# Kernel optimization log

Hardware: AMD Instinct MI355X
Metric: run time of the kernel (lower is better)

## Reference

```python
import jax, jax.numpy as jnp
import numpy as np

D_MODEL = 1024
N_HEADS = 16
HEAD_DIM = D_MODEL // N_HEADS
D_FF = 4096


def setup_inputs() -> dict:
    key = jax.random.key(0)
    ks = jax.random.split(key, 16)
    s = 0.02
    x = jax.random.normal(ks[0], (4, 2048, D_MODEL), dtype=jnp.float32)
    p = {
        'x': x,
        'wq': jax.random.normal(ks[1], (D_MODEL, D_MODEL), jnp.float32) * s,
        'bq': jnp.zeros((D_MODEL,), jnp.float32),
        'wk': jax.random.normal(ks[2], (D_MODEL, D_MODEL), jnp.float32) * s,
        'bk': jnp.zeros((D_MODEL,), jnp.float32),
        'wv': jax.random.normal(ks[3], (D_MODEL, D_MODEL), jnp.float32) * s,
        'bv': jnp.zeros((D_MODEL,), jnp.float32),
        'wo': jax.random.normal(ks[4], (D_MODEL, D_MODEL), jnp.float32) * s,
        'bo': jnp.zeros((D_MODEL,), jnp.float32),
        'w1': jax.random.normal(ks[5], (D_MODEL, D_FF), jnp.float32) * s,
        'b1': jnp.zeros((D_FF,), jnp.float32),
        'w2': jax.random.normal(ks[6], (D_FF, D_MODEL), jnp.float32) * s,
        'b2': jnp.zeros((D_MODEL,), jnp.float32),
        'ln1_g': jnp.ones((D_MODEL,), jnp.float32),
        'ln1_b': jnp.zeros((D_MODEL,), jnp.float32),
        'ln2_g': jnp.ones((D_MODEL,), jnp.float32),
        'ln2_b': jnp.zeros((D_MODEL,), jnp.float32),
    }
    return p


def _layernorm(x, g, b, eps=1e-5):
    mu = jnp.mean(x, axis=-1, keepdims=True)
    var = jnp.mean(jnp.square(x - mu), axis=-1, keepdims=True)
    return (x - mu) * jax.lax.rsqrt(var + eps) * g + b


def reference(x, wq, bq, wk, bk, wv, bv, wo, bo, w1, b1, w2, b2, ln1_g, ln1_b, ln2_g, ln2_b):
    B, S, D = x.shape
    normed = _layernorm(x, ln1_g, ln1_b)
    # projections -> [B, H, S, Dh]
    def split_heads(t):
        return t.reshape(B, S, N_HEADS, HEAD_DIM).transpose(0, 2, 1, 3)
    q = split_heads(normed @ wq + bq)
    k = split_heads(normed @ wk + bk)
    v = split_heads(normed @ wv + bv)
    scale = 1.0 / jnp.sqrt(jnp.float32(HEAD_DIM))
    scores = jnp.einsum('bhqd,bhkd->bhqk', q, k) * scale  # [B,H,S,S]
    causal = jnp.tril(jnp.ones((S, S), dtype=bool))
    scores = jnp.where(causal[None, None], scores, -jnp.inf)
    probs = jax.nn.softmax(scores, axis=-1)
    attn = jnp.einsum('bhqk,bhkd->bhqd', probs, v)
    attn = attn.transpose(0, 2, 1, 3).reshape(B, S, D)
    x = x + (attn @ wo + bo)
    h = _layernorm(x, ln2_g, ln2_b)
    h = jax.nn.gelu(h @ w1 + b1, approximate=False)
    x = x + (h @ w2 + b2)
    return x
```

## Files before the change

### kernel.cpp

```cpp
#include <hip/hip_runtime.h>
#include <hip/hip_bf16.h>
#include <math.h>

typedef __attribute__((ext_vector_type(8))) short short8;
typedef __attribute__((ext_vector_type(4))) float floatx4;

#define D_MODEL 1024
#define N_HEADS 16
#define HEAD_DIM 64
#define D_FF 4096
#define BATCH 4
#define SEQ 2048
#define NTOK (BATCH * SEQ)

#define GLOBAL_AS __attribute__((address_space(1)))
#define LDS_AS __attribute__((address_space(3)))

__device__ __forceinline__ void async_ld16(const void* g, void* l) {
    __builtin_amdgcn_global_load_lds((GLOBAL_AS const unsigned int*)g,
                                     (LDS_AS unsigned int*)l, 16, 0, 0);
}

__global__ void wtrans_kernel(const float* __restrict__ in, __hip_bfloat16* __restrict__ out,
                              int R, int C) {
    __shared__ float tile[32][33];
    const int c0 = blockIdx.x * 32, r0 = blockIdx.y * 32;
    const int tx = threadIdx.x & 31, ty = threadIdx.x >> 5;
#pragma unroll
    for (int i = 0; i < 4; ++i) {
        int r = ty + i * 8;
        tile[r][tx] = in[(size_t)(r0 + r) * C + c0 + tx];
    }
    __syncthreads();
#pragma unroll
    for (int i = 0; i < 4; ++i) {
        int r = ty + i * 8;
        out[(size_t)(c0 + r) * R + r0 + tx] = __float2bfloat16(tile[tx][r]);
    }
}

__global__ void bconcat_kernel(const float* __restrict__ bq, const float* __restrict__ bk,
                               const float* __restrict__ bv, float* __restrict__ out) {
    const int i = blockIdx.x * 256 + threadIdx.x;
    float v = (i < 1024) ? bq[i] : (i < 2048 ? bk[i - 1024] : bv[i - 2048]);
    out[i] = v;
}

__global__ void vtrans_kernel(const __hip_bfloat16* __restrict__ in,
                              __hip_bfloat16* __restrict__ out) {
    __shared__ short T[64 * 64];
    const int tid = threadIdx.x;
    const int bh = blockIdx.y;
    const int s0 = blockIdx.x * 64;
    const int4* src = (const int4*)(in + (size_t)bh * SEQ * 64 + (size_t)s0 * 64);
#pragma unroll
    for (int i = 0; i < 2; ++i) {
        int idx = i * 256 + tid;
        int s = idx >> 3, g = idx & 7;
        *(int4*)&T[s * 64 + ((g ^ (s & 7)) * 8)] = src[idx];
    }
    __syncthreads();
    const int dh = tid & 63;
    const int sgb = tid >> 6;
#pragma unroll
    for (int i = 0; i < 2; ++i) {
        const int sg = sgb + i * 4;
        short8 vv;
#pragma unroll
        for (int j = 0; j < 8; ++j) {
            const int s = sg * 8 + j;
            vv[j] = T[s * 64 + (((dh >> 3) ^ j) * 8) + (dh & 7)];
        }
        *(short8*)((short*)out + (size_t)bh * 64 * SEQ + (size_t)dh * SEQ + s0 + sg * 8) = vv;
    }
}

__global__ void ln_kernel(const float* __restrict__ x, const float* __restrict__ g,
                          const float* __restrict__ b, __hip_bfloat16* __restrict__ out) {
    const int row = blockIdx.x;
    const int tid = threadIdx.x;
    const float4 v = ((const float4*)(x + (size_t)row * D_MODEL))[tid];
    float s = v.x + v.y + v.z + v.w;
    float s2 = v.x * v.x + v.y * v.y + v.z * v.z + v.w * v.w;
#pragma unroll
    for (int off = 32; off >= 1; off >>= 1) {
        s += __shfl_xor(s, off, 64);
        s2 += __shfl_xor(s2, off, 64);
    }
    __shared__ float ss[4], ss2[4];
    const int wid = tid >> 6, lane = tid & 63;
    if (lane == 0) { ss[wid] = s; ss2[wid] = s2; }
    __syncthreads();
    const float tot = ss[0] + ss[1] + ss[2] + ss[3];
    const float tot2 = ss2[0] + ss2[1] + ss2[2] + ss2[3];
    const float mu = tot * (1.0f / D_MODEL);
    const float var = tot2 * (1.0f / D_MODEL) - mu * mu;
    const float rsq = rsqrtf(var + 1e-5f);
    const float vv[4] = {v.x, v.y, v.z, v.w};
#pragma unroll
    for (int j = 0; j < 4; ++j) {
        int c = tid * 4 + j;
        out[(size_t)row * D_MODEL + c] = __float2bfloat16((vv[j] - mu) * rsq * g[c] + b[c]);
    }
}

#define BM 128
#define BN 128
#define BK 32

template <int MODE>
__global__ void gemm_kernel(const __hip_bfloat16* __restrict__ A,
                            const __hip_bfloat16* __restrict__ Bt,
                            const float* __restrict__ bias,
                            const float* __restrict__ resid,
                            void* __restrict__ outp, int M, int N, int K, float scale) {
    __shared__ __hip_bfloat16 As[BM * BK];
    __shared__ __hip_bfloat16 Bs[BN * BK];
    const int tid = threadIdx.x;
    const int lane = tid & 63;
    const int wid = tid >> 6;
    const int wm = wid >> 1, wn = wid & 1;
    const int m0 = blockIdx.y * BM;
    const int n0 = blockIdx.x * BN;

    const size_t a_base = (size_t)(m0 + wid * 32 + (lane >> 2)) * K + (lane & 3) * 8;
    const size_t b_base = (size_t)(n0 + wid * 32 + (lane >> 2)) * K + (lane & 3) * 8;
    __hip_bfloat16* asd0 = &As[(wid * 32) * BK];
    __hip_bfloat16* asd1 = &As[(wid * 32 + 16) * BK];
    __hip_bfloat16* bsd0 = &Bs[(wid * 32) * BK];
    __hip_bfloat16* bsd1 = &Bs[(wid * 32 + 16) * BK];

    const floatx4 vzero = {0.f, 0.f, 0.f, 0.f};
    floatx4 acc[4][4];
#pragma unroll
    for (int i = 0; i < 4; ++i)
#pragma unroll
        for (int j = 0; j < 4; ++j) acc[i][j] = vzero;

    const int arow = wm * 64 + (lane & 15);
    const int brow = wn * 64 + (lane & 15);
    const int koff = (lane >> 4) * 8;

    for (int kt = 0; kt < K; kt += BK) {
        __syncthreads();
        async_ld16(A + a_base + kt, asd0);
        async_ld16(A + a_base + kt + (size_t)16 * K, asd1);
        async_ld16(Bt + b_base + kt, bsd0);
        async_ld16(Bt + b_base + kt + (size_t)16 * K, bsd1);
        __syncthreads();
        short8 af[4], bf[4];
#pragma unroll
        for (int mt = 0; mt < 4; ++mt) af[mt] = *(const short8*)&As[(arow + mt * 16) * BK + koff];
#pragma unroll
        for (int nt = 0; nt < 4; ++nt) bf[nt] = *(const short8*)&Bs[(brow + nt * 16) * BK + koff];
#pragma unroll
        for (int mt = 0; mt < 4; ++mt)
#pragma unroll
            for (int nt = 0; nt < 4; ++nt)
                acc[mt][nt] = __builtin_amdgcn_mfma_f32_16x16x32_bf16(af[mt], bf[nt], acc[mt][nt], 0, 0, 0);
    }

    const int lrow4 = (lane >> 4) * 4;
    const int lcol = lane & 15;
#pragma unroll
    for (int mt = 0; mt < 4; ++mt) {
#pragma unroll
        for (int nt = 0; nt < 4; ++nt) {
#pragma unroll
            for (int r = 0; r < 4; ++r) {
                const int gm = m0 + wm * 64 + mt * 16 + lrow4 + r;
                const int gn = n0 + wn * 64 + nt * 16 + lcol;
                float v = acc[mt][nt][r] + bias[gn];
                if (MODE == 0) {
                    const int which = gn >> 10;
                    const int rest = gn & 1023;
                    if (which == 0) v *= scale;
                    const int bb = gm >> 11, s = gm & (SEQ - 1);
                    const int h = rest >> 6, dh = rest & (HEAD_DIM - 1);
                    ((__hip_bfloat16*)outp)[(size_t)which * NTOK * D_MODEL +
                        ((size_t)(bb * N_HEADS + h) * SEQ + s) * HEAD_DIM + dh] =
                        __float2bfloat16(v);
                } else if (MODE == 1) {
                    v += resid[(size_t)gm * N + gn];
                    ((float*)outp)[(size_t)gm * N + gn] = v;
                } else if (MODE == 2) {
                    const float ge = 0.5f * v * (1.0f + erff(v * 0.70710678118654752f));
                    ((__hip_bfloat16*)outp)[(size_t)gm * N + gn] = __float2bfloat16(ge);
                } else {
                    v += resid[(size_t)gm * N + gn];
                    ((float*)outp)[(size_t)gm * N + gn] = v;
                }
            }
        }
    }
}

__global__ void attn_kernel(const __hip_bfloat16* __restrict__ q,
                            const __hip_bfloat16* __restrict__ k,
                            const __hip_bfloat16* __restrict__ vt,
                            __hip_bfloat16* __restrict__ o) {
    __shared__ __hip_bfloat16 Ks[2][64 * 64];
    __shared__ __hip_bfloat16 VTs[2][64 * 64];
    __shared__ __hip_bfloat16 Ps[4][32 * 72];

    const int tid = threadIdx.x;
    const int lane = tid & 63;
    const int w = tid >> 6;
    const int bh = blockIdx.y;
    const int b = bh >> 4, h = bh & 15;
    const int qt = (blockIdx.x + (blockIdx.y >> 2)) & 15;
    const int q0 = qt * 128;
    const size_t hb = (size_t)bh * SEQ * HEAD_DIM;
    const size_t vhb = (size_t)bh * HEAD_DIM * SEQ;

    const int lcol = lane & 15;
    const int quad = lane >> 4;
    const int koff = quad * 8;
    const int lrow4 = quad * 4;
    const int srow = lane >> 3;
    const int lgrp = (lane & 7) ^ srow;

    short8 aq[2][2];
#pragma unroll
    for (int rb = 0; rb < 2; ++rb)
#pragma unroll
        for (int ks = 0; ks < 2; ++ks)
            aq[rb][ks] = *(const short8*)(q + hb +
                (size_t)(q0 + w * 32 + rb * 16 + lcol) * 64 + ks * 32 + koff);

    const floatx4 vzero = {0.f, 0.f, 0.f, 0.f};
    floatx4 ao[2][4];
    floatx4 aol[2];
#pragma unroll
    for (int rb = 0; rb < 2; ++rb) {
        aol[rb] = vzero;
#pragma unroll
        for (int nt = 0; nt < 4; ++nt) ao[rb][nt] = vzero;
    }
    short8 vone;
#pragma unroll
    for (int j = 0; j < 8; ++j) vone[j] = (short)0x3F80;

    const int qmax_wave = q0 + w * 32 + 31;

    for (int kv0 = 0; kv0 < q0 + 128; kv0 += 128) {
        __syncthreads();
#pragma unroll
        for (int sub = 0; sub < 2; ++sub)
#pragma unroll
            for (int j = 0; j < 2; ++j) {
                const int rr = w * 16 + j * 8 + srow;
                async_ld16(k + hb + (size_t)(kv0 + sub * 64 + rr) * 64 + lgrp * 8,
                           &Ks[sub][(w * 16 + j * 8) * 64]);
                async_ld16(vt + vhb + (size_t)rr * SEQ + kv0 + sub * 64 + lgrp * 8,
                           &VTs[sub][(w * 16 + j * 8) * 64]);
            }
        __syncthreads();

#pragma unroll
        for (int sub = 0; sub < 2; ++sub) {
            const int kvb = kv0 + sub * 64;
            if (kvb > qmax_wave) continue;

            floatx4 sc[2][4];
#pragma unroll
            for (int rb = 0; rb < 2; ++rb)
#pragma unroll
                for (int nt = 0; nt < 4; ++nt) sc[rb][nt] = vzero;
#pragma unroll
            for (int nt = 0; nt < 4; ++nt) {
                const int krow = nt * 16 + lcol;
                const short8 bk0 = *(const short8*)&Ks[sub][krow * 64 + ((quad ^ (lcol & 7)) * 8)];
                const short8 bk1 = *(const short8*)&Ks[sub][krow * 64 + (((4 + quad) ^ (lcol & 7)) * 8)];
#pragma unroll
                for (int rb = 0; rb < 2; ++rb) {
                    sc[rb][nt] = __builtin_amdgcn_mfma_f32_16x16x32_bf16(aq[rb][0], bk0, sc[rb][nt], 0, 0, 0);
                    sc[rb][nt] = __builtin_amdgcn_mfma_f32_16x16x32_bf16(aq[rb][1], bk1, sc[rb][nt], 0, 0, 0);
                }
            }
            if (kvb + 63 > q0 + w * 32) {
#pragma unroll
                for (int rb = 0; rb < 2; ++rb)
#pragma unroll
                    for (int nt = 0; nt < 4; ++nt)
#pragma unroll
                        for (int r = 0; r < 4; ++r) {
                            const int qrow = q0 + w * 32 + rb * 16 + lrow4 + r;
                            const int kcol = kvb + nt * 16 + lcol;
                            if (kcol > qrow) sc[rb][nt][r] = -1e30f;
                        }
            }
#pragma unroll
            for (int rb = 0; rb < 2; ++rb)
#pragma unroll
                for (int nt = 0; nt < 4; ++nt)
#pragma unroll
                    for (int r = 0; r < 4; ++r)
                        Ps[w][(rb * 16 + lrow4 + r) * 72 + nt * 16 + lcol] =
                            __float2bfloat16(exp2f(sc[rb][nt][r]));
#pragma unroll
            for (int ks = 0; ks < 2; ++ks) {
                short8 vbf[4];
#pragma unroll
                for (int nt = 0; nt < 4; ++nt)
                    vbf[nt] = *(const short8*)&VTs[sub][(nt * 16 + lcol) * 64 +
                                                       ((((ks * 4) + quad) ^ (lcol & 7)) * 8)];
#pragma unroll
                for (int rb = 0; rb < 2; ++rb) {
                    const short8 pa = *(const short8*)&Ps[w][(rb * 16 + lcol) * 72 + ks * 32 + koff];
                    aol[rb] = __builtin_amdgcn_mfma_f32_16x16x32_bf16(pa, vone, aol[rb], 0, 0, 0);
#pragma unroll
                    for (int nt = 0; nt < 4; ++nt)
                        ao[rb][nt] = __builtin_amdgcn_mfma_f32_16x16x32_bf16(pa, vbf[nt], ao[rb][nt], 0, 0, 0);
                }
            }
        }
    }
#pragma unroll
    for (int rb = 0; rb < 2; ++rb)
#pragma unroll
        for (int nt = 0; nt < 4; ++nt)
#pragma unroll
            for (int r = 0; r < 4; ++r) {
                const int qrow = q0 + w * 32 + rb * 16 + lrow4 + r;
                const float ov = ao[rb][nt][r] / aol[rb][r];
                o[((size_t)(b * SEQ) + qrow) * D_MODEL + h * HEAD_DIM + nt * 16 + lcol] =
                    __float2bfloat16(ov);
            }
}

extern "C" void kernel_launch(void* const* d_in, const int* in_sizes, int n_in,
                              void* d_out, int out_size, void* d_ws, size_t ws_size,
                              hipStream_t stream) {
    (void)in_sizes; (void)n_in; (void)out_size; (void)ws_size;
    const float* x    = (const float*)d_in[0];
    const float* wq   = (const float*)d_in[1];
    const float* bq   = (const float*)d_in[2];
    const float* wk   = (const float*)d_in[3];
    const float* bk   = (const float*)d_in[4];
    const float* wv   = (const float*)d_in[5];
    const float* bv   = (const float*)d_in[6];
    const float* wo   = (const float*)d_in[7];
    const float* bo   = (const float*)d_in[8];
    const float* w1   = (const float*)d_in[9];
    const float* b1   = (const float*)d_in[10];
    const float* w2   = (const float*)d_in[11];
    const float* b2   = (const float*)d_in[12];
    const float* ln1g = (const float*)d_in[13];
    const float* ln1b = (const float*)d_in[14];
    const float* ln2g = (const float*)d_in[15];
    const float* ln2b = (const float*)d_in[16];
    float* out = (float*)d_out;

    char* ws = (char*)d_ws;
    size_t off = 0;
    auto alloc = [&](size_t bytes) { void* p = ws + off; off += bytes; return p; };
    __hip_bfloat16* wqkvT = (__hip_bfloat16*)alloc((size_t)3072 * 1024 * 2);
    __hip_bfloat16* woT = (__hip_bfloat16*)alloc((size_t)1024 * 1024 * 2);
    __hip_bfloat16* w1T = (__hip_bfloat16*)alloc((size_t)4096 * 1024 * 2);
    __hip_bfloat16* w2T = (__hip_bfloat16*)alloc((size_t)4096 * 1024 * 2);
    float* bqkv = (float*)alloc((size_t)3072 * 4);
    __hip_bfloat16* normed = (__hip_bfloat16*)alloc((size_t)NTOK * D_MODEL * 2);
    __hip_bfloat16* qb = (__hip_bfloat16*)alloc((size_t)NTOK * D_MODEL * 2);
    __hip_bfloat16* kb = (__hip_bfloat16*)alloc((size_t)NTOK * D_MODEL * 2);
    __hip_bfloat16* vb = (__hip_bfloat16*)alloc((size_t)NTOK * D_MODEL * 2);
    __hip_bfloat16* attnb = (__hip_bfloat16*)alloc((size_t)NTOK * D_MODEL * 2);
    float* x1 = (float*)alloc((size_t)NTOK * D_MODEL * 4);
    __hip_bfloat16* hh = (__hip_bfloat16*)alloc((size_t)NTOK * D_FF * 2);
    __hip_bfloat16* vtb = (__hip_bfloat16*)hh;

    const float QSCALE = 0.125f * 1.44269504088896f;

    const dim3 blk(256);
    wtrans_kernel<<<dim3(32, 32), blk, 0, stream>>>(wq, wqkvT, 1024, 1024);
    wtrans_kernel<<<dim3(32, 32), blk, 0, stream>>>(wk, wqkvT + (size_t)1024 * 1024, 1024, 1024);
    wtrans_kernel<<<dim3(32, 32), blk, 0, stream>>>(wv, wqkvT + (size_t)2048 * 1024, 1024, 1024);
    wtrans_kernel<<<dim3(32, 32), blk, 0, stream>>>(wo, woT, 1024, 1024);
    wtrans_kernel<<<dim3(128, 32), blk, 0, stream>>>(w1, w1T, 1024, 4096);
    wtrans_kernel<<<dim3(32, 128), blk, 0, stream>>>(w2, w2T, 4096, 1024);
    bconcat_kernel<<<dim3(12), blk, 0, stream>>>(bq, bk, bv, bqkv);

    ln_kernel<<<NTOK, blk, 0, stream>>>(x, ln1g, ln1b, normed);

    gemm_kernel<0><<<dim3(3072 / BN, NTOK / BM), blk, 0, stream>>>(normed, wqkvT, bqkv, nullptr, qb, NTOK, 3072, 1024, QSCALE);

    vtrans_kernel<<<dim3(SEQ / 64, BATCH * N_HEADS), blk, 0, stream>>>(vb, vtb);

    attn_kernel<<<dim3(SEQ / 128, BATCH * N_HEADS), blk, 0, stream>>>(qb, kb, vtb, attnb);

    gemm_kernel<1><<<dim3(1024 / BN, NTOK / BM), blk, 0, stream>>>(attnb, woT, bo, x, x1, NTOK, 1024, 1024, 1.0f);

    ln_kernel<<<NTOK, blk, 0, stream>>>(x1, ln2g, ln2b, normed);

    gemm_kernel<2><<<dim3(D_FF / BN, NTOK / BM), blk, 0, stream>>>(normed, w1T, b1, nullptr, hh, NTOK, D_FF, 1024, 1.0f);
    gemm_kernel<3><<<dim3(1024 / BN, NTOK / BM), blk, 0, stream>>>(hh, w2T, b2, x1, out, NTOK, 1024, D_FF, 1.0f);
}
```

Baseline: 589.1 us.

## Double GEMM K-tile to 64 with XOR-swizzled LDS layout and swapped grid order

Raises the GEMM K tile from 32 to 64 so each pair of barriers covers twice as many MFMA steps, halving the synchronisation count per unit of work. Global-to-LDS async loads now use an XOR swizzle of the 16-byte column group by row, matched on the read side, to avoid LDS bank conflicts with the wider rows. The grid is transposed so M tiles vary fastest, changing which blocks run together and so the L2 reuse of A and B tiles. LDS use doubles to 32 KB per block, which may reduce occupancy.

```diff
diff --git a/kernel.cpp b/kernel.cpp
--- a/kernel.cpp
+++ b/kernel.cpp
@@ -106,7 +106,7 @@
 
 #define BM 128
 #define BN 128
-#define BK 32
+#define BK 64
 
 template <int MODE>
 __global__ void gemm_kernel(const __hip_bfloat16* __restrict__ A,
@@ -118,17 +118,16 @@
     __shared__ __hip_bfloat16 Bs[BN * BK];
     const int tid = threadIdx.x;
     const int lane = tid & 63;
-    const int wid = tid >> 6;
-    const int wm = wid >> 1, wn = wid & 1;
-    const int m0 = blockIdx.y * BM;
-    const int n0 = blockIdx.x * BN;
-
-    const size_t a_base = (size_t)(m0 + wid * 32 + (lane >> 2)) * K + (lane & 3) * 8;
-    const size_t b_base = (size_t)(n0 + wid * 32 + (lane >> 2)) * K + (lane & 3) * 8;
-    __hip_bfloat16* asd0 = &As[(wid * 32) * BK];
-    __hip_bfloat16* asd1 = &As[(wid * 32 + 16) * BK];
-    __hip_bfloat16* bsd0 = &Bs[(wid * 32) * BK];
-    __hip_bfloat16* bsd1 = &Bs[(wid * 32 + 16) * BK];
+    const int w = tid >> 6;
+    const int wm = w >> 1, wn = w & 1;
+    const int m0 = blockIdx.x * BM;
+    const int n0 = blockIdx.y * BN;
+
+    const int srow = lane >> 3;
+    const int lgrp = (lane & 7) ^ srow;
+
+    const size_t a_base = (size_t)(m0 + w * 32 + srow) * K + lgrp * 8;
+    const size_t b_base = (size_t)(n0 + w * 32 + srow) * K + lgrp * 8;
 
     const floatx4 vzero = {0.f, 0.f, 0.f, 0.f};
     floatx4 acc[4][4];
@@ -137,31 +136,38 @@
 #pragma unroll
         for (int j = 0; j < 4; ++j) acc[i][j] = vzero;
 
-    const int arow = wm * 64 + (lane & 15);
-    const int brow = wn * 64 + (lane & 15);
-    const int koff = (lane >> 4) * 8;
+    const int lcol = lane & 15;
+    const int quad = lane >> 4;
+    const int arow = wm * 64 + lcol;
+    const int brow = wn * 64 + lcol;
+    const int l7 = lcol & 7;
 
     for (int kt = 0; kt < K; kt += BK) {
         __syncthreads();
-        async_ld16(A + a_base + kt, asd0);
-        async_ld16(A + a_base + kt + (size_t)16 * K, asd1);
-        async_ld16(Bt + b_base + kt, bsd0);
-        async_ld16(Bt + b_base + kt + (size_t)16 * K, bsd1);
+#pragma unroll
+        for (int j = 0; j < 4; ++j)
+            async_ld16(A + a_base + kt + (size_t)(j * 8) * K, &As[(w * 32 + j * 8) * BK]);
+#pragma unroll
+        for (int j = 0; j < 4; ++j)
+            async_ld16(Bt + b_base + kt + (size_t)(j * 8) * K, &Bs[(w * 32 + j * 8) * BK]);
         __syncthreads();
-        short8 af[4], bf[4];
-#pragma unroll
-        for (int mt = 0; mt < 4; ++mt) af[mt] = *(const short8*)&As[(arow + mt * 16) * BK + koff];
-#pragma unroll
-        for (int nt = 0; nt < 4; ++nt) bf[nt] = *(const short8*)&Bs[(brow + nt * 16) * BK + koff];
-#pragma unroll
-        for (int mt = 0; mt < 4; ++mt)
-#pragma unroll
-            for (int nt = 0; nt < 4; ++nt)
-                acc[mt][nt] = __builtin_amdgcn_mfma_f32_16x16x32_bf16(af[mt], bf[nt], acc[mt][nt], 0, 0, 0);
-    }
-
-    const int lrow4 = (lane >> 4) * 4;
-    const int lcol = lane & 15;
+#pragma unroll
+        for (int ks = 0; ks < 2; ++ks) {
+            const int g = ((ks * 4 + quad) ^ l7) * 8;
+            short8 af[4], bf[4];
+#pragma unroll
+            for (int mt = 0; mt < 4; ++mt) af[mt] = *(const short8*)&As[(arow + mt * 16) * BK + g];
+#pragma unroll
+            for (int nt = 0; nt < 4; ++nt) bf[nt] = *(const short8*)&Bs[(brow + nt * 16) * BK + g];
+#pragma unroll
+            for (int mt = 0; mt < 4; ++mt)
+#pragma unroll
+                for (int nt = 0; nt < 4; ++nt)
+                    acc[mt][nt] = __builtin_amdgcn_mfma_f32_16x16x32_bf16(af[mt], bf[nt], acc[mt][nt], 0, 0, 0);
+        }
+    }
+
+    const int lrow4 = quad * 4;
 #pragma unroll
     for (int mt = 0; mt < 4; ++mt) {
 #pragma unroll
@@ -382,16 +388,16 @@
 
     ln_kernel<<<NTOK, blk, 0, stream>>>(x, ln1g, ln1b, normed);
 
-    gemm_kernel<0><<<dim3(3072 / BN, NTOK / BM), blk, 0, stream>>>(normed, wqkvT, bqkv, nullptr, qb, NTOK, 3072, 1024, QSCALE);
+    gemm_kernel<0><<<dim3(NTOK / BM, 3072 / BN), blk, 0, stream>>>(normed, wqkvT, bqkv, nullptr, qb, NTOK, 3072, 1024, QSCALE);
 
     vtrans_kernel<<<dim3(SEQ / 64, BATCH * N_HEADS), blk, 0, stream>>>(vb, vtb);
 
     attn_kernel<<<dim3(SEQ / 128, BATCH * N_HEADS), blk, 0, stream>>>(qb, kb, vtb, attnb);
 
-    gemm_kernel<1><<<dim3(1024 / BN, NTOK / BM), blk, 0, stream>>>(attnb, woT, bo, x, x1, NTOK, 1024, 1024, 1.0f);
+    gemm_kernel<1><<<dim3(NTOK / BM, 1024 / BN), blk, 0, stream>>>(attnb, woT, bo, x, x1, NTOK, 1024, 1024, 1.0f);
 
     ln_kernel<<<NTOK, blk, 0, stream>>>(x1, ln2g, ln2b, normed);
 
-    gemm_kernel<2><<<dim3(D_FF / BN, NTOK / BM), blk, 0, stream>>>(normed, w1T, b1, nullptr, hh, NTOK, D_FF, 1024, 1.0f);
-    gemm_kernel<3><<<dim3(1024 / BN, NTOK / BM), blk, 0, stream>>>(hh, w2T, b2, x1, out, NTOK, 1024, D_FF, 1.0f);
-}
+    gemm_kernel<2><<<dim3(NTOK / BM, D_FF / BN), blk, 0, stream>>>(normed, w1T, b1, nullptr, hh, NTOK, D_FF, 1024, 1.0f);
+    gemm_kernel<3><<<dim3(NTOK / BM, 1024 / BN), blk, 0, stream>>>(hh, w2T, b2, x1, out, NTOK, 1024, D_FF, 1.0f);
+}
```

Result: faster. 544.7 us (-7.5%).
